# Performance work log

Hardware: AMD Instinct MI355X
Metric: run time of the kernel (lower is better)

The kernel has to match this reference:

```python
import jax, jax.numpy as jnp
import numpy as np

E = 20000
EDGE_DIM = 16
CH_IN = 32
CH_OUT = 32
T_IN = 1
T_OUT = 1
D_IN = 2 * T_IN + 1      # 3
D_OUT = 2 * T_OUT + 1    # 3
NUM_FREQ = 2 * min(T_IN, T_OUT) + 1  # 3
EPS = 1e-5


def setup_inputs() -> dict:
    key = jax.random.key(0)
    ks = jax.random.split(key, 6)
    return {
        "f": jax.random.normal(ks[0], (E, EDGE_DIM + 1), dtype=jnp.float32),
        "basis": jax.random.normal(ks[1], (E, 1, D_OUT, 1, D_IN, NUM_FREQ), dtype=jnp.float32),
        "w1": jax.random.normal(ks[2], (32, EDGE_DIM + 1), dtype=jnp.float32) * (2.0 / (EDGE_DIM + 1)) ** 0.5,
        "b1": jnp.zeros((32,), jnp.float32),
        "g1": jnp.ones((32,), jnp.float32),
        "be1": jnp.zeros((32,), jnp.float32),
        "w2": jax.random.normal(ks[3], (32, 32), dtype=jnp.float32) * (2.0 / 32) ** 0.5,
        "b2": jnp.zeros((32,), jnp.float32),
        "g2": jnp.ones((32,), jnp.float32),
        "be2": jnp.zeros((32,), jnp.float32),
        "w3": jax.random.normal(ks[4], (NUM_FREQ * CH_IN * CH_OUT, 32), dtype=jnp.float32) * (2.0 / 32) ** 0.5,
        "b3": jnp.zeros((NUM_FREQ * CH_IN * CH_OUT,), jnp.float32),
    }


def _layernorm(x, g, b):
    mu = jnp.mean(x, axis=-1, keepdims=True)
    var = jnp.mean(jnp.square(x - mu), axis=-1, keepdims=True)
    return (x - mu) * jax.lax.rsqrt(var + EPS) * g + b


def reference(f, basis, w1, b1, g1, be1, w2, b2, g2, be2, w3, b3):
    # Radial MLP: Linear -> LN -> ReLU -> Linear -> LN -> ReLU -> Linear
    h = jax.nn.relu(_layernorm(f @ w1.T + b1, g1, be1))
    h = jax.nn.relu(_layernorm(h @ w2.T + b2, g2, be2))
    r = h @ w3.T + b3                                 # [E, ch_out*ch_in*num_freq]
    R = r.reshape(E, CH_OUT, CH_IN, NUM_FREQ)
    B = basis.reshape(E, D_OUT, D_IN, NUM_FREQ)       # squeeze broadcast dims
    # contraction over num_freq without the (E,co,do,ci,di,nf) blowup
    kernel = jnp.einsum('ecdf,epqf->ecpdq', R, B)     # [E, ch_out, d_out, ch_in, d_in]
    return kernel.reshape(E, D_OUT * CH_OUT, CH_IN * D_IN)
```

## Files before the change

kernel.cpp:

```cpp
#include <hip/hip_runtime.h>

#define EB 4
#define NT 384
#define W3STRIDE 36

__global__ __launch_bounds__(NT) void singleconv_fused(
    const float* __restrict__ f,
    const float* __restrict__ basis,
    const float* __restrict__ w1,
    const float* __restrict__ b1,
    const float* __restrict__ g1,
    const float* __restrict__ be1,
    const float* __restrict__ w2,
    const float* __restrict__ b2,
    const float* __restrict__ g2,
    const float* __restrict__ be2,
    const float* __restrict__ w3,
    const float* __restrict__ b3,
    float* __restrict__ out)
{
    __shared__ float sf[EB][17];
    __shared__ float sbas[EB][27];
    __shared__ float sh1[EB][32];
    __shared__ alignas(16) float sh2[EB][32];
    __shared__ float smu[EB], srs[EB];
    __shared__ alignas(16) float sw3[96 * W3STRIDE];
    __shared__ float sr[EB * 96];

    const int t  = threadIdx.x;
    const int e0 = blockIdx.x * EB;

    if (t < EB * 17) {
        int e = t / 17, i = t - e * 17;
        sf[e][i] = f[(e0 + e) * 17 + i];
    }
    if (t >= 128 && t < 128 + EB * 27) {
        int q = t - 128;
        int e = q / 27, i = q - e * 27;
        sbas[e][i] = basis[(e0 + e) * 27 + i];
    }
    __syncthreads();

    if (t < EB * 32) {
        int e = t >> 5, j = t & 31;
        float acc = b1[j];
        #pragma unroll
        for (int k = 0; k < 17; k++) acc += sf[e][k] * w1[j * 17 + k];
        sh1[e][j] = acc;
    }
    __syncthreads();
    if (t < EB) {
        float mu = 0.f;
        #pragma unroll
        for (int j = 0; j < 32; j++) mu += sh1[t][j];
        mu *= (1.f / 32.f);
        float var = 0.f;
        #pragma unroll
        for (int j = 0; j < 32; j++) { float d = sh1[t][j] - mu; var += d * d; }
        var *= (1.f / 32.f);
        smu[t] = mu; srs[t] = rsqrtf(var + 1e-5f);
    }
    __syncthreads();
    if (t < EB * 32) {
        int e = t >> 5, j = t & 31;
        float y = (sh1[e][j] - smu[e]) * srs[e] * g1[j] + be1[j];
        sh1[e][j] = fmaxf(y, 0.f);
    }
    __syncthreads();

    if (t < EB * 32) {
        int e = t >> 5, j = t & 31;
        float acc = b2[j];
        #pragma unroll
        for (int k = 0; k < 32; k++) acc += sh1[e][k] * w2[j * 32 + k];
        sh2[e][j] = acc;
    }
    __syncthreads();
    if (t < EB) {
        float mu = 0.f;
        #pragma unroll
        for (int j = 0; j < 32; j++) mu += sh2[t][j];
        mu *= (1.f / 32.f);
        float var = 0.f;
        #pragma unroll
        for (int j = 0; j < 32; j++) { float d = sh2[t][j] - mu; var += d * d; }
        var *= (1.f / 32.f);
        smu[t] = mu; srs[t] = rsqrtf(var + 1e-5f);
    }
    __syncthreads();
    if (t < EB * 32) {
        int e = t >> 5, j = t & 31;
        float y = (sh2[e][j] - smu[e]) * srs[e] * g2[j] + be2[j];
        sh2[e][j] = fmaxf(y, 0.f);
    }
    __syncthreads();

    const int re   = t / 96;
    const int rcol = t - re * 96;
    const int wrow = t >> 2;
    const int wk   = (t & 3) * 8;

    int ep_srb[3], ep_sbb[3], ep_off[3], ep_row[3];
    #pragma unroll
    for (int s = 0; s < 3; s++) {
        int idx  = t + s * NT;
        int e    = idx / 288;
        int rem  = idx - e * 288;
        int dord = rem / 96;
        int c    = rem - dord * 96;
        int ci   = c / 3;
        int di   = c - ci * 3;
        ep_srb[s] = e * 96 + ci * 3;
        ep_sbb[s] = e * 27 + dord * 9 + di * 3;
        ep_row[s] = dord;
        ep_off[s] = (e0 + e) * 9216 + c;
    }
    const float* sbf = &sbas[0][0];

    for (int co = 0; co < 32; co++) {
        __syncthreads();

        {
            const float4* wsrc = (const float4*)(w3 + co * 3072);
            float4 a = wsrc[t * 2];
            float4 b = wsrc[t * 2 + 1];
            float* wd = &sw3[wrow * W3STRIDE + wk];
            *(float4*)(wd)     = a;
            *(float4*)(wd + 4) = b;
        }
        __syncthreads();

        {
            float acc = b3[co * 96 + rcol];
            const float* wp = &sw3[rcol * W3STRIDE];
            const float* hp = &sh2[re][0];
            #pragma unroll
            for (int k = 0; k < 32; k += 4) {
                float4 w = *(const float4*)(wp + k);
                float4 h = *(const float4*)(hp + k);
                acc += w.x * h.x + w.y * h.y + w.z * h.z + w.w * h.w;
            }
            sr[t] = acc;
        }
        __syncthreads();

        #pragma unroll
        for (int s = 0; s < 3; s++) {
            const float* rp = &sr[ep_srb[s]];
            const float* bp = sbf + ep_sbb[s];
            float v = rp[0] * bp[0] + rp[1] * bp[1] + rp[2] * bp[2];
            out[ep_off[s] + (co * 3 + ep_row[s]) * 96] = v;
        }
    }
}

extern "C" void kernel_launch(void* const* d_in, const int* in_sizes, int n_in,
                              void* d_out, int out_size, void* d_ws, size_t ws_size,
                              hipStream_t stream) {
    const float* f     = (const float*)d_in[0];
    const float* basis = (const float*)d_in[1];
    const float* w1    = (const float*)d_in[2];
    const float* b1    = (const float*)d_in[3];
    const float* g1    = (const float*)d_in[4];
    const float* be1   = (const float*)d_in[5];
    const float* w2    = (const float*)d_in[6];
    const float* b2    = (const float*)d_in[7];
    const float* g2    = (const float*)d_in[8];
    const float* be2   = (const float*)d_in[9];
    const float* w3    = (const float*)d_in[10];
    const float* b3    = (const float*)d_in[11];
    float* out = (float*)d_out;

    dim3 grid(20000 / EB), block(NT);
    hipLaunchKernelGGL(singleconv_fused, grid, block, 0, stream,
                       f, basis, w1, b1, g1, be1, w2, b2, g2, be2, w3, b3, out);
}
```

Measured before the change: 909.8 us.

## Prefetch w3 into double-buffered shared memory and vectorize epilogue stores

Register-prefetches the next co slice of w3 and b3 while computing the current one, using double-buffered shared memory so only two barriers remain per iteration. LayerNorm statistics now come from warp shuffles instead of single-thread serial loops, which removes several barriers. Each thread keeps its h2 row and basis block in registers and writes three contiguous outputs in one store per iteration. The trade-off is higher register pressure and twice the w3 shared memory, and the loop issues one redundant wrapped prefetch on its last iteration.

```diff
diff --git a/kernel.cpp b/kernel.cpp
--- a/kernel.cpp
+++ b/kernel.cpp
@@ -2,7 +2,9 @@
 
 #define EB 4
 #define NT 384
-#define W3STRIDE 36
+#define W3S 36
+
+struct F3 { float x, y, z; };
 
 __global__ __launch_bounds__(NT) void singleconv_fused(
     const float* __restrict__ f,
@@ -23,20 +25,28 @@
     __shared__ float sbas[EB][27];
     __shared__ float sh1[EB][32];
     __shared__ alignas(16) float sh2[EB][32];
-    __shared__ float smu[EB], srs[EB];
-    __shared__ alignas(16) float sw3[96 * W3STRIDE];
+    __shared__ alignas(16) float sw3[2][96 * W3S];
     __shared__ float sr[EB * 96];
 
     const int t  = threadIdx.x;
     const int e0 = blockIdx.x * EB;
 
-    if (t < EB * 17) {
-        int e = t / 17, i = t - e * 17;
-        sf[e][i] = f[(e0 + e) * 17 + i];
+    const int re   = t / 96;
+    const int rcol = t - re * 96;
+    const int wrow = t >> 2;
+    const int wk   = (t & 3) * 8;
+
+    float4 pa, pb;
+    {
+        const float4* ws = (const float4*)(w3);
+        pa = ws[t * 2];
+        pb = ws[t * 2 + 1];
     }
+    float bnx = b3[rcol];
+
+    if (t < EB * 17) { int e = t / 17, i = t - e * 17; sf[e][i] = f[(e0 + e) * 17 + i]; }
     if (t >= 128 && t < 128 + EB * 27) {
-        int q = t - 128;
-        int e = q / 27, i = q - e * 27;
+        int q = t - 128, e = q / 27, i = q - e * 27;
         sbas[e][i] = basis[(e0 + e) * 27 + i];
     }
     __syncthreads();
@@ -46,25 +56,16 @@
         float acc = b1[j];
         #pragma unroll
         for (int k = 0; k < 17; k++) acc += sf[e][k] * w1[j * 17 + k];
-        sh1[e][j] = acc;
-    }
-    __syncthreads();
-    if (t < EB) {
-        float mu = 0.f;
+        float s = acc;
         #pragma unroll
-        for (int j = 0; j < 32; j++) mu += sh1[t][j];
-        mu *= (1.f / 32.f);
-        float var = 0.f;
+        for (int m = 16; m >= 1; m >>= 1) s += __shfl_xor(s, m);
+        float mu = s * (1.f / 32.f);
+        float d  = acc - mu;
+        float v  = d * d;
         #pragma unroll
-        for (int j = 0; j < 32; j++) { float d = sh1[t][j] - mu; var += d * d; }
-        var *= (1.f / 32.f);
-        smu[t] = mu; srs[t] = rsqrtf(var + 1e-5f);
-    }
-    __syncthreads();
-    if (t < EB * 32) {
-        int e = t >> 5, j = t & 31;
-        float y = (sh1[e][j] - smu[e]) * srs[e] * g1[j] + be1[j];
-        sh1[e][j] = fmaxf(y, 0.f);
+        for (int m = 16; m >= 1; m >>= 1) v += __shfl_xor(v, m);
+        float rs = rsqrtf(v * (1.f / 32.f) + 1e-5f);
+        sh1[e][j] = fmaxf(d * rs * g1[j] + be1[j], 0.f);
     }
     __syncthreads();
 
@@ -73,84 +74,70 @@
         float acc = b2[j];
         #pragma unroll
         for (int k = 0; k < 32; k++) acc += sh1[e][k] * w2[j * 32 + k];
-        sh2[e][j] = acc;
-    }
-    __syncthreads();
-    if (t < EB) {
-        float mu = 0.f;
+        float s = acc;
         #pragma unroll
-        for (int j = 0; j < 32; j++) mu += sh2[t][j];
-        mu *= (1.f / 32.f);
-        float var = 0.f;
+        for (int m = 16; m >= 1; m >>= 1) s += __shfl_xor(s, m);
+        float mu = s * (1.f / 32.f);
+        float d  = acc - mu;
+        float v  = d * d;
         #pragma unroll
-        for (int j = 0; j < 32; j++) { float d = sh2[t][j] - mu; var += d * d; }
-        var *= (1.f / 32.f);
-        smu[t] = mu; srs[t] = rsqrtf(var + 1e-5f);
-    }
-    __syncthreads();
-    if (t < EB * 32) {
-        int e = t >> 5, j = t & 31;
-        float y = (sh2[e][j] - smu[e]) * srs[e] * g2[j] + be2[j];
-        sh2[e][j] = fmaxf(y, 0.f);
+        for (int m = 16; m >= 1; m >>= 1) v += __shfl_xor(v, m);
+        float rs = rsqrtf(v * (1.f / 32.f) + 1e-5f);
+        sh2[e][j] = fmaxf(d * rs * g2[j] + be2[j], 0.f);
     }
     __syncthreads();
 
-    const int re   = t / 96;
-    const int rcol = t - re * 96;
-    const int wrow = t >> 2;
-    const int wk   = (t & 3) * 8;
+    float4 hv[8];
+    {
+        const float4* hp = (const float4*)(&sh2[re][0]);
+        #pragma unroll
+        for (int k = 0; k < 8; k++) hv[k] = hp[k];
+    }
 
-    int ep_srb[3], ep_sbb[3], ep_off[3], ep_row[3];
-    #pragma unroll
-    for (int s = 0; s < 3; s++) {
-        int idx  = t + s * NT;
-        int e    = idx / 288;
-        int rem  = idx - e * 288;
-        int dord = rem / 96;
-        int c    = rem - dord * 96;
-        int ci   = c / 3;
-        int di   = c - ci * 3;
-        ep_srb[s] = e * 96 + ci * 3;
-        ep_sbb[s] = e * 27 + dord * 9 + di * 3;
-        ep_row[s] = dord;
-        ep_off[s] = (e0 + e) * 9216 + c;
+    const int dord = rcol >> 5;
+    const int ci   = t & 31;
+    float br[3][3];
+    {
+        const float* bp = &sbas[re][dord * 9];
+        #pragma unroll
+        for (int q = 0; q < 9; q++) (&br[0][0])[q] = bp[q];
     }
-    const float* sbf = &sbas[0][0];
+    const float* rp = &sr[re * 96 + ci * 3];
+    float* op = out + (size_t)(e0 + re) * 9216 + dord * 96 + ci * 3;
 
-    for (int co = 0; co < 32; co++) {
+    int buf = 0;
+    for (int co = 0; co < 32; ++co) {
+        float* wd = &sw3[buf][wrow * W3S + wk];
+        *(float4*)(wd)     = pa;
+        *(float4*)(wd + 4) = pb;
+        float bcur = bnx;
+
+        int cn = (co + 1) & 31;
+        const float4* ws = (const float4*)(w3 + cn * 3072);
+        pa  = ws[t * 2];
+        pb  = ws[t * 2 + 1];
+        bnx = b3[cn * 96 + rcol];
+
         __syncthreads();
 
-        {
-            const float4* wsrc = (const float4*)(w3 + co * 3072);
-            float4 a = wsrc[t * 2];
-            float4 b = wsrc[t * 2 + 1];
-            float* wd = &sw3[wrow * W3STRIDE + wk];
-            *(float4*)(wd)     = a;
-            *(float4*)(wd + 4) = b;
+        float acc = bcur;
+        const float* wp = &sw3[buf][rcol * W3S];
+        #pragma unroll
+        for (int k = 0; k < 8; k++) {
+            float4 w = *(const float4*)(wp + k * 4);
+            acc += w.x * hv[k].x + w.y * hv[k].y + w.z * hv[k].z + w.w * hv[k].w;
         }
+        sr[t] = acc;
         __syncthreads();
 
-        {
-            float acc = b3[co * 96 + rcol];
-            const float* wp = &sw3[rcol * W3STRIDE];
-            const float* hp = &sh2[re][0];
-            #pragma unroll
-            for (int k = 0; k < 32; k += 4) {
-                float4 w = *(const float4*)(wp + k);
-                float4 h = *(const float4*)(hp + k);
-                acc += w.x * h.x + w.y * h.y + w.z * h.z + w.w * h.w;
-            }
-            sr[t] = acc;
-        }
-        __syncthreads();
+        float r0 = rp[0], r1 = rp[1], r2 = rp[2];
+        F3 o;
+        o.x = r0 * br[0][0] + r1 * br[0][1] + r2 * br[0][2];
+        o.y = r0 * br[1][0] + r1 * br[1][1] + r2 * br[1][2];
+        o.z = r0 * br[2][0] + r1 * br[2][1] + r2 * br[2][2];
+        *(F3*)(op + co * 288) = o;
 
-        #pragma unroll
-        for (int s = 0; s < 3; s++) {
-            const float* rp = &sr[ep_srb[s]];
-            const float* bp = sbf + ep_sbb[s];
-            float v = rp[0] * bp[0] + rp[1] * bp[1] + rp[2] * bp[2];
-            out[ep_off[s] + (co * 3 + ep_row[s]) * 96] = v;
-        }
+        buf ^= 1;
     }
 }
 
```

After: 858.4 us. -5.6%, faster.
